# Performance work log

Measured on AMD Instinct MI355X. Metric: run time of the kernel, lower is better.

Reference implementation:

```python
import jax, jax.numpy as jnp
import numpy as np

N_WIRES = 4
N_OPS = 20

# Deterministic surrogate for tq.RandomLayer(n_ops=20): fixed random op list.
_rng = np.random.default_rng(1234)
OPS = []
for _i in range(N_OPS):
    kind = ['rx', 'ry', 'rz', 'cnot'][int(_rng.integers(4))]
    w = int(_rng.integers(N_WIRES))
    OPS.append((kind, w))

C64 = jnp.complex64

def _ry(theta):
    c = jnp.cos(theta / 2).astype(C64)
    s = jnp.sin(theta / 2).astype(C64)
    return jnp.stack([jnp.stack([c, -s], -1), jnp.stack([s, c], -1)], -2)

def _rx(theta):
    c = jnp.cos(theta / 2).astype(C64)
    s = jnp.sin(theta / 2).astype(C64)
    return jnp.stack([jnp.stack([c, -1j * s], -1), jnp.stack([-1j * s, c], -1)], -2)

def _rz(theta):
    e0 = jnp.exp(-1j * theta.astype(C64) / 2)
    e1 = jnp.exp(1j * theta.astype(C64) / 2)
    z = jnp.zeros_like(e0)
    return jnp.stack([jnp.stack([e0, z], -1), jnp.stack([z, e1], -1)], -2)

_CNOT = jnp.array([[1, 0, 0, 0], [0, 1, 0, 0], [0, 0, 0, 1], [0, 0, 1, 0]],
                  dtype=C64).reshape(2, 2, 2, 2)

def _apply_1q(state, gate, w):
    # state: (N,2,2,2,2); gate: (2,2) or (N,2,2)
    s = jnp.moveaxis(state, 1 + w, -1)
    if gate.ndim == 2:
        s = jnp.einsum('ij,n...j->n...i', gate, s)
    else:
        s = jnp.einsum('nij,n...j->n...i', gate, s)
    return jnp.moveaxis(s, -1, 1 + w)

def _apply_2q(state, gate4, c, t):
    s = jnp.moveaxis(state, (1 + c, 1 + t), (-2, -1))
    s = jnp.einsum('abcd,n...cd->n...ab', gate4, s)
    return jnp.moveaxis(s, (-2, -1), (1 + c, 1 + t))

def quantum_layer(vec, rand_angles, rx_theta, ry_theta):
    # vec: (N, 4) real angles. Returns (N, 4) PauliZ expectations.
    n = vec.shape[0]
    state = jnp.zeros((n, 2 ** N_WIRES), C64).at[:, 0].set(1.0)
    state = state.reshape((n,) + (2,) * N_WIRES)
    # GeneralEncoder '4xRy': RY(vec[:, w]) on each wire (batched angles)
    for w in range(N_WIRES):
        state = _apply_1q(state, _ry(vec[:, w]), w)
    # RandomLayer surrogate
    for i, (kind, w) in enumerate(OPS):
        th = rand_angles[i]
        if kind == 'rx':
            state = _apply_1q(state, _rx(th), w)
        elif kind == 'ry':
            state = _apply_1q(state, _ry(th), w)
        elif kind == 'rz':
            state = _apply_1q(state, _rz(th), w)
        else:
            state = _apply_2q(state, _CNOT, w, (w + 1) % N_WIRES)
    # Trainable RX/RY (single shared param each), applied on every wire
    gx, gy = _rx(rx_theta), _ry(ry_theta)
    for w in range(N_WIRES):
        state = _apply_1q(state, gx, w)
        state = _apply_1q(state, gy, w)
    # MeasureAll PauliZ
    probs = state.real ** 2 + state.imag ** 2  # (N,2,2,2,2)
    zs = []
    for w in range(N_WIRES):
        axes = tuple(a for a in range(1, 1 + N_WIRES) if a != 1 + w)
        m = probs.sum(axis=axes)  # (N, 2)
        zs.append(m[:, 0] - m[:, 1])
    return jnp.stack(zs, -1)

def _apply_quantum(t, rand_angles, rx_theta, ry_theta):
    # t: (B, H, T, D) -> elementwise per-(b,h,t) quantum transform
    B, H, T, D = t.shape
    out = quantum_layer(t.reshape(B * H * T, D), rand_angles, rx_theta, ry_theta)
    return out.reshape(B, H, T, D)

def setup_inputs() -> dict:
    key = jax.random.key(0)
    ks = jax.random.split(key, 7)
    B, T, C = 4, 2048, 256
    H, D = 64, 4
    x = jax.random.normal(ks[0], (B, T, C), jnp.float32)
    w_qkv = jax.random.normal(ks[1], (3 * C, C), jnp.float32) * (1.0 / np.sqrt(C))
    w_out = jax.random.normal(ks[2], (C, C), jnp.float32) * (1.0 / np.sqrt(C))
    b_out = jnp.zeros((C,), jnp.float32)
    rx_theta = jax.random.uniform(ks[3], (), jnp.float32, 0.0, 2 * np.pi)
    ry_theta = jax.random.uniform(ks[4], (), jnp.float32, 0.0, 2 * np.pi)
    rand_angles = jax.random.uniform(ks[5], (N_OPS,), jnp.float32, 0.0, 2 * np.pi)
    return {'x': x, 'w_qkv': w_qkv, 'w_out': w_out, 'b_out': b_out,
            'rx_theta': rx_theta, 'ry_theta': ry_theta, 'rand_angles': rand_angles}

def reference(x, w_qkv, w_out, b_out, rx_theta, ry_theta, rand_angles):
    B, T, C = x.shape
    H, D = 64, 4
    qkv = (x @ w_qkv.T).reshape(B, T, 3, H, D).transpose(2, 0, 3, 1, 4)
    q, k, v = qkv[0], qkv[1], qkv[2]  # each (B, H, T, D)
    q = _apply_quantum(q, rand_angles, rx_theta, ry_theta)
    k = _apply_quantum(k, rand_angles, rx_theta, ry_theta)
    v = _apply_quantum(v, rand_angles, rx_theta, ry_theta)
    # Faithful to original einsum labels: q,k,v are (B,H,T,D) so 't','s' index heads
    scores = jnp.einsum('bthd,bshd->bths', q, k) / (D ** 0.5)  # (B,H,T,H)
    attn = jax.nn.softmax(scores, axis=-1)  # dropout is eval-mode identity
    out = jnp.einsum('bths,bshd->bthd', attn, v)  # (B,H,T,D)
    out = out.reshape(B, T, C)  # faithful memory-layout reshape as in original
    return out @ w_out.T + b_out
```

## Files before the change

kernel.cpp:

```cpp
#include <hip/hip_runtime.h>
#include <stdint.h>
#include <stddef.h>

typedef __attribute__((ext_vector_type(8))) short short8;
typedef __attribute__((ext_vector_type(4))) float floatx4;

static void compute_ops_host(int* kinds, int* wires) {
  const uint32_t MULT_A = 0x931e8875u;
  const uint32_t INIT_B = 0x8b51f9ddu, MULT_B = 0x58f38dedu;
  const uint32_t MIX_L = 0xca01f9ddu, MIX_R = 0x4973f715u;
  uint32_t hc = 0x43b0d7e5u;
  auto hashmix = [&](uint32_t v) -> uint32_t {
    v ^= hc; hc *= MULT_A; v *= hc; v ^= v >> 16; return v;
  };
  auto mix = [&](uint32_t x, uint32_t y) -> uint32_t {
    uint32_t r = (x * MIX_L) - (y * MIX_R); r ^= r >> 16; return r;
  };
  uint32_t pool[4];
  for (int i = 0; i < 4; ++i) pool[i] = hashmix(i == 0 ? 1234u : 0u);
  for (int s = 0; s < 4; ++s)
    for (int d = 0; d < 4; ++d)
      if (s != d) pool[d] = mix(pool[d], hashmix(pool[s]));
  uint32_t st32[8];
  uint32_t hcb = INIT_B;
  for (int i = 0; i < 8; ++i) {
    uint32_t dv = pool[i & 3];
    dv ^= hcb; hcb *= MULT_B; dv *= hcb; dv ^= dv >> 16;
    st32[i] = dv;
  }
  uint64_t s64[4];
  for (int k = 0; k < 4; ++k) s64[k] = (uint64_t)st32[2 * k] | ((uint64_t)st32[2 * k + 1] << 32);
  const __uint128_t M = ((__uint128_t)0x2360ed051fc65da4ULL << 64) | 0x4385df649fccf645ULL;
  __uint128_t initstate = ((__uint128_t)s64[0] << 64) | s64[1];
  __uint128_t inc = ((((__uint128_t)s64[2] << 64) | s64[3]) << 1) | (__uint128_t)1;
  __uint128_t state = inc;
  state += initstate;
  state = state * M + inc;
  bool has = false; uint32_t hbuf = 0;
  auto next32 = [&]() -> uint32_t {
    if (has) { has = false; return hbuf; }
    state = state * M + inc;
    uint64_t hi = (uint64_t)(state >> 64), lo = (uint64_t)state;
    uint64_t x = hi ^ lo;
    unsigned rot = (unsigned)(state >> 122) & 63u;
    uint64_t o = (x >> rot) | (x << ((64u - rot) & 63u));
    has = true; hbuf = (uint32_t)(o >> 32);
    return (uint32_t)o;
  };
  for (int i = 0; i < 20; ++i) {
    kinds[i] = (int)(((uint64_t)next32() * 4ull) >> 32);
    wires[i] = (int)(((uint64_t)next32() * 4ull) >> 32);
  }
}

__global__ __launch_bounds__(256) void build_tables(
    const float* __restrict__ rand_angles, const float* __restrict__ rx_theta,
    const float* __restrict__ ry_theta, unsigned long long kinds,
    unsigned long long wires, float* __restrict__ Tg)
{
  __shared__ float Ur[16][16], Ui[16][16];
  __shared__ float Msh[4][16][16];
  const int tid = threadIdx.x;
  {
    int i = tid >> 4, j = tid & 15;
    Ur[i][j] = (i == j) ? 1.0f : 0.0f;
    Ui[i][j] = 0.0f;
  }
  __syncthreads();
  for (int g = 0; g < 28; ++g) {
    int kind, w; float th;
    if (g < 20) {
      kind = (int)((kinds >> (2 * g)) & 3ull);
      w = (int)((wires >> (2 * g)) & 3ull);
      th = rand_angles[g];
    } else {
      int e = g - 20;
      w = e >> 1;
      kind = (e & 1) ? 1 : 0;
      th = (e & 1) ? ry_theta[0] : rx_theta[0];
    }
    if (kind == 3) {
      int mc = 8 >> w, mt = 8 >> ((w + 1) & 3);
      if (tid < 64) {
        int pi = tid >> 4, j = tid & 15;
        int i = mc, pbit = 0;
        for (int b = 3; b >= 0; --b) {
          int mask = 1 << b;
          if (mask != mc && mask != mt) { i |= ((pi >> pbit) & 1) << b; pbit++; }
        }
        int i2 = i | mt;
        float tr = Ur[i][j], ti = Ui[i][j];
        Ur[i][j] = Ur[i2][j]; Ui[i][j] = Ui[i2][j];
        Ur[i2][j] = tr; Ui[i2][j] = ti;
      }
    } else {
      float s, c;
      sincosf(th * 0.5f, &s, &c);
      float g00r, g00i, g01r, g01i, g10r, g10i, g11r, g11i;
      if (kind == 0) {
        g00r = c; g00i = 0; g01r = 0; g01i = -s; g10r = 0; g10i = -s; g11r = c; g11i = 0;
      } else if (kind == 1) {
        g00r = c; g00i = 0; g01r = -s; g01i = 0; g10r = s; g10i = 0; g11r = c; g11i = 0;
      } else {
        g00r = c; g00i = -s; g01r = 0; g01i = 0; g10r = 0; g10i = 0; g11r = c; g11i = s;
      }
      if (tid < 128) {
        int p = tid >> 4, j = tid & 15;
        int mb = 3 - w;
        int i0 = ((p >> mb) << (mb + 1)) | (p & ((1 << mb) - 1));
        int i1 = i0 | (1 << mb);
        float ar = Ur[i0][j], ai = Ui[i0][j];
        float br = Ur[i1][j], bi = Ui[i1][j];
        Ur[i0][j] = g00r * ar - g00i * ai + g01r * br - g01i * bi;
        Ui[i0][j] = g00r * ai + g00i * ar + g01r * bi + g01i * br;
        Ur[i1][j] = g10r * ar - g10i * ai + g11r * br - g11i * bi;
        Ui[i1][j] = g10r * ai + g10i * ar + g11r * bi + g11i * br;
      }
    }
    __syncthreads();
  }
  {
    int j = tid >> 4, k = tid & 15;
    float m0 = 0, m1 = 0, m2 = 0, m3 = 0;
#pragma unroll
    for (int l = 0; l < 16; ++l) {
      float p = Ur[l][j] * Ur[l][k] + Ui[l][j] * Ui[l][k];
      m0 += (l & 8) ? -p : p;
      m1 += (l & 4) ? -p : p;
      m2 += (l & 2) ? -p : p;
      m3 += (l & 1) ? -p : p;
    }
    Msh[0][j][k] = m0; Msh[1][j][k] = m1; Msh[2][j][k] = m2; Msh[3][j][k] = m3;
  }
  __syncthreads();
  if (tid < 81) {
    int e4 = tid % 3, r = tid / 3;
    int ee0 = r / 9, ee1 = (r / 3) % 3, ee2 = r % 3;
    int ee[4] = { ee0, ee1, ee2, e4 };
    float s0 = 0, s1 = 0, s2 = 0, s3 = 0;
    for (int m = 0; m < 16; ++m) {
      int j = 0, k = 0; float coef = 1.0f;
      for (int i = 0; i < 4; ++i) {
        int o = (m >> i) & 1;
        int e = ee[i];
        int bj, bk; float c;
        if (e == 2)      { bj = o; bk = 1 - o; c = 0.5f; }
        else if (e == 1) { bj = o; bk = o;     c = o ? -0.5f : 0.5f; }
        else             { bj = o; bk = o;     c = 0.5f; }
        j |= bj << (3 - i); k |= bk << (3 - i);
        coef *= c;
      }
      s0 += coef * Msh[0][j][k]; s1 += coef * Msh[1][j][k];
      s2 += coef * Msh[2][j][k]; s3 += coef * Msh[3][j][k];
    }
    Tg[(0 * 27 + r) * 4 + e4] = s0;
    Tg[(1 * 27 + r) * 4 + e4] = s1;
    Tg[(2 * 27 + r) * 4 + e4] = s2;
    Tg[(3 * 27 + r) * 4 + e4] = s3;
  }
  if (tid >= 81 && tid < 108) {
    int r = tid - 81;
    for (int w = 0; w < 4; ++w) Tg[(w * 27 + r) * 4 + 3] = 0.0f;
  }
}

static __device__ __forceinline__ unsigned short bf16_rn(float x) {
  uint32_t u = __float_as_uint(x);
  return (unsigned short)((u + 0x7FFFu + ((u >> 16) & 1u)) >> 16);
}
static __device__ __forceinline__ void split2(float x, unsigned short& h, unsigned short& l) {
  h = bf16_rn(x);
  float hf = __uint_as_float(((uint32_t)h) << 16);
  l = bf16_rn(x - hf);
}

__global__ __launch_bounds__(256) void conv_split_all(
    const float* __restrict__ x, unsigned short* __restrict__ xh, unsigned short* __restrict__ xl,
    const float* __restrict__ wq, unsigned short* __restrict__ wh, unsigned short* __restrict__ wl,
    const float* __restrict__ wo, unsigned short* __restrict__ woh, unsigned short* __restrict__ wol)
{
  int bid = blockIdx.x;
  const float* in; unsigned short *h, *l; int i;
  if (bid < 2048)      { in = x;  h = xh;  l = xl;  i = bid * 256 + threadIdx.x; }
  else if (bid < 2240) { in = wq; h = wh;  l = wl;  i = (bid - 2048) * 256 + threadIdx.x; }
  else                 { in = wo; h = woh; l = wol; i = (bid - 2240) * 256 + threadIdx.x; }
  float4 v = *reinterpret_cast<const float4*>(&in[(size_t)i * 4]);
  ushort4 hh, ll;
  split2(v.x, hh.x, ll.x);
  split2(v.y, hh.y, ll.y);
  split2(v.z, hh.z, ll.z);
  split2(v.w, hh.w, ll.w);
  *reinterpret_cast<ushort4*>(&h[(size_t)i * 4]) = hh;
  *reinterpret_cast<ushort4*>(&l[(size_t)i * 4]) = ll;
}

__global__ __launch_bounds__(256) void gemm_bf16s(
    const unsigned short* __restrict__ Ah, const unsigned short* __restrict__ Al,
    const unsigned short* __restrict__ Bh, const unsigned short* __restrict__ Bl,
    const float* __restrict__ bias, float* __restrict__ C,
    int M, int N, int K, int nbx)
{
  __shared__ __align__(16) unsigned short sAh[128 * 64];
  __shared__ __align__(16) unsigned short sAl[128 * 64];
  __shared__ __align__(16) unsigned short sBh[64 * 64];
  __shared__ __align__(16) unsigned short sBl[64 * 64];
  int cpx = gridDim.x >> 3;
  int wg = (blockIdx.x & 7) * cpx + (blockIdx.x >> 3);
  const int bx = wg % nbx, by = wg / nbx;
  const int bm = by * 128, bn = bx * 64;
  const int tid = threadIdx.x;
  const int wave = tid >> 6, lane = tid & 63;
  const int wm = wave >> 1, wn = wave & 1;
  const int fr = lane & 15, fg = lane >> 4;
  floatx4 acc[4][2] = {};
  for (int k0 = 0; k0 < K; k0 += 64) {
    __syncthreads();
#pragma unroll
    for (int rd = 0; rd < 4; ++rd) {
      int idx = tid + rd * 256;
      int row = idx >> 3, s = idx & 7;
      int ss = s ^ (row & 7);
      size_t go = (size_t)(bm + row) * K + k0 + s * 8;
      *reinterpret_cast<uint4*>(&sAh[(row * 8 + ss) * 8]) =
          *reinterpret_cast<const uint4*>(&Ah[go]);
      *reinterpret_cast<uint4*>(&sAl[(row * 8 + ss) * 8]) =
          *reinterpret_cast<const uint4*>(&Al[go]);
    }
#pragma unroll
    for (int rd = 0; rd < 2; ++rd) {
      int idx = tid + rd * 256;
      int row = idx >> 3, s = idx & 7;
      int ss = s ^ (row & 7);
      size_t go = (size_t)(bn + row) * K + k0 + s * 8;
      *reinterpret_cast<uint4*>(&sBh[(row * 8 + ss) * 8]) =
          *reinterpret_cast<const uint4*>(&Bh[go]);
      *reinterpret_cast<uint4*>(&sBl[(row * 8 + ss) * 8]) =
          *reinterpret_cast<const uint4*>(&Bl[go]);
    }
    __syncthreads();
#pragma unroll
    for (int kk = 0; kk < 2; ++kk) {
      short8 a_h[4], a_l[4], b_h[2], b_l[2];
#pragma unroll
      for (int fm = 0; fm < 4; ++fm) {
        int row = wm * 64 + fm * 16 + fr;
        int ss = (kk * 4 + fg) ^ (row & 7);
        a_h[fm] = *reinterpret_cast<const short8*>(&sAh[(row * 8 + ss) * 8]);
        a_l[fm] = *reinterpret_cast<const short8*>(&sAl[(row * 8 + ss) * 8]);
      }
#pragma unroll
      for (int fn = 0; fn < 2; ++fn) {
        int row = wn * 32 + fn * 16 + fr;
        int ss = (kk * 4 + fg) ^ (row & 7);
        b_h[fn] = *reinterpret_cast<const short8*>(&sBh[(row * 8 + ss) * 8]);
        b_l[fn] = *reinterpret_cast<const short8*>(&sBl[(row * 8 + ss) * 8]);
      }
#pragma unroll
      for (int fm = 0; fm < 4; ++fm)
#pragma unroll
        for (int fn = 0; fn < 2; ++fn) {
          acc[fm][fn] = __builtin_amdgcn_mfma_f32_16x16x32_bf16(a_h[fm], b_h[fn], acc[fm][fn], 0, 0, 0);
          acc[fm][fn] = __builtin_amdgcn_mfma_f32_16x16x32_bf16(a_h[fm], b_l[fn], acc[fm][fn], 0, 0, 0);
          acc[fm][fn] = __builtin_amdgcn_mfma_f32_16x16x32_bf16(a_l[fm], b_h[fn], acc[fm][fn], 0, 0, 0);
        }
    }
  }
#pragma unroll
  for (int fm = 0; fm < 4; ++fm) {
    int rowb = bm + wm * 64 + fm * 16 + fg * 4;
#pragma unroll
    for (int fn = 0; fn < 2; ++fn) {
      int col = bn + wn * 32 + fn * 16 + fr;
      float bv = (bias != nullptr) ? bias[col] : 0.0f;
#pragma unroll
      for (int r = 0; r < 4; ++r)
        C[(size_t)(rowb + r) * N + col] = acc[fm][fn][r] + bv;
    }
  }
}

__global__ __launch_bounds__(256) void quantum_apply1(
    float* __restrict__ p0, const float* __restrict__ Tg)
{
  size_t base = ((size_t)blockIdx.x * 256 + threadIdx.x) * 4;
  float4 A = *reinterpret_cast<const float4*>(&p0[base]);
  float cv[4], sv[4];
  __sincosf(A.x, &sv[0], &cv[0]);
  __sincosf(A.y, &sv[1], &cv[1]);
  __sincosf(A.z, &sv[2], &cv[2]);
  __sincosf(A.w, &sv[3], &cv[3]);
  float z[4];
#pragma unroll
  for (int w = 0; w < 4; ++w) {
    float a1_ = 0.f;
#pragma unroll
    for (int e1 = 0; e1 < 3; ++e1) {
      float a2_ = 0.f;
#pragma unroll
      for (int e2 = 0; e2 < 3; ++e2) {
        float a3_ = 0.f;
#pragma unroll
        for (int e3 = 0; e3 < 3; ++e3) {
          const float4 t4 = *reinterpret_cast<const float4*>(
              &Tg[(w * 27 + e1 * 9 + e2 * 3 + e3) * 4]);
          float inner = fmaf(sv[3], t4.z, fmaf(cv[3], t4.y, t4.x));
          if (e3 == 0)      a3_ += inner;
          else if (e3 == 1) a3_ = fmaf(inner, cv[2], a3_);
          else              a3_ = fmaf(inner, sv[2], a3_);
        }
        if (e2 == 0)      a2_ += a3_;
        else if (e2 == 1) a2_ = fmaf(a3_, cv[1], a2_);
        else              a2_ = fmaf(a3_, sv[1], a2_);
      }
      if (e1 == 0)      a1_ += a2_;
      else if (e1 == 1) a1_ = fmaf(a2_, cv[0], a1_);
      else              a1_ = fmaf(a2_, sv[0], a1_);
    }
    z[w] = a1_;
  }
  *reinterpret_cast<float4*>(&p0[base]) = make_float4(z[0], z[1], z[2], z[3]);
}

static __device__ __forceinline__ float rl(float x, int l) {
  return __int_as_float(__builtin_amdgcn_readlane(__float_as_int(x), l));
}

__global__ __launch_bounds__(256) void attn_rl_b(
    const float* __restrict__ qkv, unsigned short* __restrict__ yh,
    unsigned short* __restrict__ yl)
{
  const int wave = threadIdx.x >> 6, lane = threadIdx.x & 63;
  const int posIdx = blockIdx.x * 4 + wave;
  const float* row = qkv + (size_t)posIdx * 768;
  float4 q = *reinterpret_cast<const float4*>(&row[lane * 4]);
  float4 k = *reinterpret_cast<const float4*>(&row[256 + lane * 4]);
  float4 v = *reinterpret_cast<const float4*>(&row[512 + lane * 4]);
  float nx = 0, ny = 0, nz = 0, nw = 0, den = 0;
#pragma unroll
  for (int ss = 0; ss < 64; ++ss) {
    float kx = rl(k.x, ss), ky = rl(k.y, ss), kz = rl(k.z, ss), kw = rl(k.w, ss);
    float d = fmaf(q.x, kx, fmaf(q.y, ky, fmaf(q.z, kz, q.w * kw)));
    float e = __expf(d * 0.5f);
    den += e;
    nx = fmaf(e, rl(v.x, ss), nx);
    ny = fmaf(e, rl(v.y, ss), ny);
    nz = fmaf(e, rl(v.z, ss), nz);
    nw = fmaf(e, rl(v.w, ss), nw);
  }
  float inv = 1.0f / den;
  const int b = posIdx >> 11, pos = posIdx & 2047;
  size_t off = (((size_t)(b * 64 + lane)) * 2048 + pos) * 4;
  ushort4 hh, ll;
  split2(nx * inv, hh.x, ll.x);
  split2(ny * inv, hh.y, ll.y);
  split2(nz * inv, hh.z, ll.z);
  split2(nw * inv, hh.w, ll.w);
  *reinterpret_cast<ushort4*>(&yh[off]) = hh;
  *reinterpret_cast<ushort4*>(&yl[off]) = ll;
}

extern "C" void kernel_launch(void* const* d_in, const int* in_sizes, int n_in,
                              void* d_out, int out_size, void* d_ws, size_t ws_size,
                              hipStream_t stream)
{
  const float* x    = (const float*)d_in[0];
  const float* wqkv = (const float*)d_in[1];
  const float* wout = (const float*)d_in[2];
  const float* bout = (const float*)d_in[3];
  const float* rxth = (const float*)d_in[4];
  const float* ryth = (const float*)d_in[5];
  const float* rang = (const float*)d_in[6];
  float* out = (float*)d_out;

  uint8_t* w8 = (uint8_t*)d_ws;
  float* Tg = (float*)w8;
  float* p0 = (float*)(w8 + 4096);
  uint8_t* bb = w8 + 4096 + (size_t)8192 * 768 * 4;
  unsigned short* xh  = (unsigned short*)bb;
  unsigned short* xl  = xh + (size_t)8192 * 256;
  unsigned short* wh  = xl + (size_t)8192 * 256;
  unsigned short* wl  = wh + (size_t)768 * 256;
  unsigned short* woh = wl + (size_t)768 * 256;
  unsigned short* wol = woh + (size_t)256 * 256;
  unsigned short* yh  = wol + (size_t)256 * 256;
  unsigned short* yl  = yh + (size_t)8192 * 256;

  int kinds[20], wires[20];
  compute_ops_host(kinds, wires);
  unsigned long long pk = 0, pw = 0;
  for (int i = 0; i < 20; ++i) {
    pk |= (unsigned long long)(kinds[i] & 3) << (2 * i);
    pw |= (unsigned long long)(wires[i] & 3) << (2 * i);
  }

  hipLaunchKernelGGL(build_tables, dim3(1), dim3(256), 0, stream,
                     rang, rxth, ryth, pk, pw, Tg);
  hipLaunchKernelGGL(conv_split_all, dim3(2304), dim3(256), 0, stream,
                     x, xh, xl, wqkv, wh, wl, wout, woh, wol);
  hipLaunchKernelGGL(gemm_bf16s, dim3(768), dim3(256), 0, stream,
                     xh, xl, wh, wl, (const float*)nullptr, p0, 8192, 768, 256, 12);
  hipLaunchKernelGGL(quantum_apply1, dim3(6144), dim3(256), 0, stream, p0, Tg);
  hipLaunchKernelGGL(attn_rl_b, dim3(2048), dim3(256), 0, stream, p0, yh, yl);
  hipLaunchKernelGGL(gemm_bf16s, dim3(256), dim3(256), 0, stream,
                     yh, yl, woh, wol, bout, out, 8192, 256, 256, 4);
}
```

Baseline: 93.06 us.

## Fuse table build with conversion, quantum map into attention, smaller output GEMM tile

Merges the single-block table builder into the bf16 split-conversion kernel as an extra block, which removes one launch. Fuses the quantum expectation map into the attention kernel through shared memory, so the full qkv buffer is no longer read and written an extra time. Adds a 64x64-tile variant of the output GEMM, giving 512 blocks instead of 256 for better occupancy across CUs. The fused attention kernel does more per-block work and adds syncs in exchange. The extra table-build block runs concurrently with conversion, and the later kernels still depend on it through stream order.

```diff
diff --git a/kernel.cpp b/kernel.cpp
--- a/kernel.cpp
+++ b/kernel.cpp
@@ -53,14 +53,43 @@
   }
 }
 
-__global__ __launch_bounds__(256) void build_tables(
+static __device__ __forceinline__ unsigned short bf16_rn(float x) {
+  uint32_t u = __float_as_uint(x);
+  return (unsigned short)((u + 0x7FFFu + ((u >> 16) & 1u)) >> 16);
+}
+static __device__ __forceinline__ void split2(float x, unsigned short& h, unsigned short& l) {
+  h = bf16_rn(x);
+  float hf = __uint_as_float(((uint32_t)h) << 16);
+  l = bf16_rn(x - hf);
+}
+
+__global__ __launch_bounds__(256) void prep(
     const float* __restrict__ rand_angles, const float* __restrict__ rx_theta,
     const float* __restrict__ ry_theta, unsigned long long kinds,
-    unsigned long long wires, float* __restrict__ Tg)
+    unsigned long long wires, float* __restrict__ Tg,
+    const float* __restrict__ x, unsigned short* __restrict__ xh, unsigned short* __restrict__ xl,
+    const float* __restrict__ wq, unsigned short* __restrict__ wh, unsigned short* __restrict__ wl,
+    const float* __restrict__ wo, unsigned short* __restrict__ woh, unsigned short* __restrict__ wol)
 {
   __shared__ float Ur[16][16], Ui[16][16];
   __shared__ float Msh[4][16][16];
+  const int bid = blockIdx.x;
   const int tid = threadIdx.x;
+  if (bid < 2304) {
+    const float* in; unsigned short *h, *l; int i;
+    if (bid < 2048)      { in = x;  h = xh;  l = xl;  i = bid * 256 + tid; }
+    else if (bid < 2240) { in = wq; h = wh;  l = wl;  i = (bid - 2048) * 256 + tid; }
+    else                 { in = wo; h = woh; l = wol; i = (bid - 2240) * 256 + tid; }
+    float4 v = *reinterpret_cast<const float4*>(&in[(size_t)i * 4]);
+    ushort4 hh, ll;
+    split2(v.x, hh.x, ll.x);
+    split2(v.y, hh.y, ll.y);
+    split2(v.z, hh.z, ll.z);
+    split2(v.w, hh.w, ll.w);
+    *reinterpret_cast<ushort4*>(&h[(size_t)i * 4]) = hh;
+    *reinterpret_cast<ushort4*>(&l[(size_t)i * 4]) = ll;
+    return;
+  }
   {
     int i = tid >> 4, j = tid & 15;
     Ur[i][j] = (i == j) ? 1.0f : 0.0f;
@@ -164,36 +193,6 @@
   }
 }
 
-static __device__ __forceinline__ unsigned short bf16_rn(float x) {
-  uint32_t u = __float_as_uint(x);
-  return (unsigned short)((u + 0x7FFFu + ((u >> 16) & 1u)) >> 16);
-}
-static __device__ __forceinline__ void split2(float x, unsigned short& h, unsigned short& l) {
-  h = bf16_rn(x);
-  float hf = __uint_as_float(((uint32_t)h) << 16);
-  l = bf16_rn(x - hf);
-}
-
-__global__ __launch_bounds__(256) void conv_split_all(
-    const float* __restrict__ x, unsigned short* __restrict__ xh, unsigned short* __restrict__ xl,
-    const float* __restrict__ wq, unsigned short* __restrict__ wh, unsigned short* __restrict__ wl,
-    const float* __restrict__ wo, unsigned short* __restrict__ woh, unsigned short* __restrict__ wol)
-{
-  int bid = blockIdx.x;
-  const float* in; unsigned short *h, *l; int i;
-  if (bid < 2048)      { in = x;  h = xh;  l = xl;  i = bid * 256 + threadIdx.x; }
-  else if (bid < 2240) { in = wq; h = wh;  l = wl;  i = (bid - 2048) * 256 + threadIdx.x; }
-  else                 { in = wo; h = woh; l = wol; i = (bid - 2240) * 256 + threadIdx.x; }
-  float4 v = *reinterpret_cast<const float4*>(&in[(size_t)i * 4]);
-  ushort4 hh, ll;
-  split2(v.x, hh.x, ll.x);
-  split2(v.y, hh.y, ll.y);
-  split2(v.z, hh.z, ll.z);
-  split2(v.w, hh.w, ll.w);
-  *reinterpret_cast<ushort4*>(&h[(size_t)i * 4]) = hh;
-  *reinterpret_cast<ushort4*>(&l[(size_t)i * 4]) = ll;
-}
-
 __global__ __launch_bounds__(256) void gemm_bf16s(
     const unsigned short* __restrict__ Ah, const unsigned short* __restrict__ Al,
     const unsigned short* __restrict__ Bh, const unsigned short* __restrict__ Bl,
@@ -279,11 +278,88 @@
   }
 }
 
-__global__ __launch_bounds__(256) void quantum_apply1(
-    float* __restrict__ p0, const float* __restrict__ Tg)
-{
-  size_t base = ((size_t)blockIdx.x * 256 + threadIdx.x) * 4;
-  float4 A = *reinterpret_cast<const float4*>(&p0[base]);
+__global__ __launch_bounds__(256) void gemm_bf16s64(
+    const unsigned short* __restrict__ Ah, const unsigned short* __restrict__ Al,
+    const unsigned short* __restrict__ Bh, const unsigned short* __restrict__ Bl,
+    const float* __restrict__ bias, float* __restrict__ C,
+    int M, int N, int K, int nbx)
+{
+  __shared__ __align__(16) unsigned short sAh[64 * 64];
+  __shared__ __align__(16) unsigned short sAl[64 * 64];
+  __shared__ __align__(16) unsigned short sBh[64 * 64];
+  __shared__ __align__(16) unsigned short sBl[64 * 64];
+  int cpx = gridDim.x >> 3;
+  int wg = (blockIdx.x & 7) * cpx + (blockIdx.x >> 3);
+  const int bx = wg % nbx, by = wg / nbx;
+  const int bm = by * 64, bn = bx * 64;
+  const int tid = threadIdx.x;
+  const int wave = tid >> 6, lane = tid & 63;
+  const int wm = wave >> 1, wn = wave & 1;
+  const int fr = lane & 15, fg = lane >> 4;
+  floatx4 acc[2][2] = {};
+  for (int k0 = 0; k0 < K; k0 += 64) {
+    __syncthreads();
+#pragma unroll
+    for (int rd = 0; rd < 2; ++rd) {
+      int idx = tid + rd * 256;
+      int row = idx >> 3, s = idx & 7;
+      int ss = s ^ (row & 7);
+      size_t goA = (size_t)(bm + row) * K + k0 + s * 8;
+      *reinterpret_cast<uint4*>(&sAh[(row * 8 + ss) * 8]) =
+          *reinterpret_cast<const uint4*>(&Ah[goA]);
+      *reinterpret_cast<uint4*>(&sAl[(row * 8 + ss) * 8]) =
+          *reinterpret_cast<const uint4*>(&Al[goA]);
+      size_t goB = (size_t)(bn + row) * K + k0 + s * 8;
+      *reinterpret_cast<uint4*>(&sBh[(row * 8 + ss) * 8]) =
+          *reinterpret_cast<const uint4*>(&Bh[goB]);
+      *reinterpret_cast<uint4*>(&sBl[(row * 8 + ss) * 8]) =
+          *reinterpret_cast<const uint4*>(&Bl[goB]);
+    }
+    __syncthreads();
+#pragma unroll
+    for (int kk = 0; kk < 2; ++kk) {
+      short8 a_h[2], a_l[2], b_h[2], b_l[2];
+#pragma unroll
+      for (int fm = 0; fm < 2; ++fm) {
+        int row = wm * 32 + fm * 16 + fr;
+        int ss = (kk * 4 + fg) ^ (row & 7);
+        a_h[fm] = *reinterpret_cast<const short8*>(&sAh[(row * 8 + ss) * 8]);
+        a_l[fm] = *reinterpret_cast<const short8*>(&sAl[(row * 8 + ss) * 8]);
+      }
+#pragma unroll
+      for (int fn = 0; fn < 2; ++fn) {
+        int row = wn * 32 + fn * 16 + fr;
+        int ss = (kk * 4 + fg) ^ (row & 7);
+        b_h[fn] = *reinterpret_cast<const short8*>(&sBh[(row * 8 + ss) * 8]);
+        b_l[fn] = *reinterpret_cast<const short8*>(&sBl[(row * 8 + ss) * 8]);
+      }
+#pragma unroll
+      for (int fm = 0; fm < 2; ++fm)
+#pragma unroll
+        for (int fn = 0; fn < 2; ++fn) {
+          acc[fm][fn] = __builtin_amdgcn_mfma_f32_16x16x32_bf16(a_h[fm], b_h[fn], acc[fm][fn], 0, 0, 0);
+          acc[fm][fn] = __builtin_amdgcn_mfma_f32_16x16x32_bf16(a_h[fm], b_l[fn], acc[fm][fn], 0, 0, 0);
+          acc[fm][fn] = __builtin_amdgcn_mfma_f32_16x16x32_bf16(a_l[fm], b_h[fn], acc[fm][fn], 0, 0, 0);
+        }
+    }
+  }
+#pragma unroll
+  for (int fm = 0; fm < 2; ++fm) {
+    int rowb = bm + wm * 32 + fm * 16 + fg * 4;
+#pragma unroll
+    for (int fn = 0; fn < 2; ++fn) {
+      int col = bn + wn * 32 + fn * 16 + fr;
+      float bv = (bias != nullptr) ? bias[col] : 0.0f;
+#pragma unroll
+      for (int r = 0; r < 4; ++r)
+        C[(size_t)(rowb + r) * N + col] = acc[fm][fn][r] + bv;
+    }
+  }
+}
+
+static __device__ __forceinline__ float4 quantum_vec(
+    const float* __restrict__ Tg, float4 A)
+{
   float cv[4], sv[4];
   __sincosf(A.x, &sv[0], &cv[0]);
   __sincosf(A.y, &sv[1], &cv[1]);
@@ -318,23 +394,34 @@
     }
     z[w] = a1_;
   }
-  *reinterpret_cast<float4*>(&p0[base]) = make_float4(z[0], z[1], z[2], z[3]);
+  return make_float4(z[0], z[1], z[2], z[3]);
 }
 
 static __device__ __forceinline__ float rl(float x, int l) {
   return __int_as_float(__builtin_amdgcn_readlane(__float_as_int(x), l));
 }
 
-__global__ __launch_bounds__(256) void attn_rl_b(
-    const float* __restrict__ qkv, unsigned short* __restrict__ yh,
-    unsigned short* __restrict__ yl)
-{
-  const int wave = threadIdx.x >> 6, lane = threadIdx.x & 63;
-  const int posIdx = blockIdx.x * 4 + wave;
-  const float* row = qkv + (size_t)posIdx * 768;
-  float4 q = *reinterpret_cast<const float4*>(&row[lane * 4]);
-  float4 k = *reinterpret_cast<const float4*>(&row[256 + lane * 4]);
-  float4 v = *reinterpret_cast<const float4*>(&row[512 + lane * 4]);
+__global__ __launch_bounds__(256) void qattn(
+    const float* __restrict__ p0, const float* __restrict__ Tg,
+    unsigned short* __restrict__ yh, unsigned short* __restrict__ yl)
+{
+  __shared__ float qv[4][192][4];
+  const int tid = threadIdx.x;
+  const int pb = blockIdx.x * 4;
+#pragma unroll
+  for (int pass = 0; pass < 3; ++pass) {
+    int gv = pass * 256 + tid;
+    int pos = gv / 192, slot = gv - pos * 192;
+    float4 a = *reinterpret_cast<const float4*>(
+        &p0[(size_t)(pb + pos) * 768 + slot * 4]);
+    float4 z = quantum_vec(Tg, a);
+    *reinterpret_cast<float4*>(&qv[pos][slot][0]) = z;
+    __syncthreads();
+  }
+  const int wave = tid >> 6, lane = tid & 63;
+  float4 q = *reinterpret_cast<const float4*>(&qv[wave][lane][0]);
+  float4 k = *reinterpret_cast<const float4*>(&qv[wave][64 + lane][0]);
+  float4 v = *reinterpret_cast<const float4*>(&qv[wave][128 + lane][0]);
   float nx = 0, ny = 0, nz = 0, nw = 0, den = 0;
 #pragma unroll
   for (int ss = 0; ss < 64; ++ss) {
@@ -348,8 +435,9 @@
     nw = fmaf(e, rl(v.w, ss), nw);
   }
   float inv = 1.0f / den;
-  const int b = posIdx >> 11, pos = posIdx & 2047;
-  size_t off = (((size_t)(b * 64 + lane)) * 2048 + pos) * 4;
+  const int posIdx = pb + wave;
+  const int b = posIdx >> 11, pos2 = posIdx & 2047;
+  size_t off = (((size_t)(b * 64 + lane)) * 2048 + pos2) * 4;
   ushort4 hh, ll;
   split2(nx * inv, hh.x, ll.x);
   split2(ny * inv, hh.y, ll.y);
@@ -393,14 +481,12 @@
     pw |= (unsigned long long)(wires[i] & 3) << (2 * i);
   }
 
-  hipLaunchKernelGGL(build_tables, dim3(1), dim3(256), 0, stream,
-                     rang, rxth, ryth, pk, pw, Tg);
-  hipLaunchKernelGGL(conv_split_all, dim3(2304), dim3(256), 0, stream,
+  hipLaunchKernelGGL(prep, dim3(2305), dim3(256), 0, stream,
+                     rang, rxth, ryth, pk, pw, Tg,
                      x, xh, xl, wqkv, wh, wl, wout, woh, wol);
   hipLaunchKernelGGL(gemm_bf16s, dim3(768), dim3(256), 0, stream,
                      xh, xl, wh, wl, (const float*)nullptr, p0, 8192, 768, 256, 12);
-  hipLaunchKernelGGL(quantum_apply1, dim3(6144), dim3(256), 0, stream, p0, Tg);
-  hipLaunchKernelGGL(attn_rl_b, dim3(2048), dim3(256), 0, stream, p0, yh, yl);
-  hipLaunchKernelGGL(gemm_bf16s, dim3(256), dim3(256), 0, stream,
+  hipLaunchKernelGGL(qattn, dim3(2048), dim3(256), 0, stream, p0, Tg, yh, yl);
+  hipLaunchKernelGGL(gemm_bf16s64, dim3(512), dim3(256), 0, stream,
                      yh, yl, woh, wol, bout, out, 8192, 256, 256, 4);
 }
```

Result: slower. 115.7 us (+24.3%).
